# Kernel tuning notes

Hardware: AMD Instinct MI355X
Metric: run time of the kernel (lower is better)

The kernel has to match this reference:

```python
import jax, jax.numpy as jnp
import numpy as np

K = 20
EPS = 1e-5


def _knn_idx(x, k):
    # x: (B, C, N) -> idx (B, N, k) of nearest neighbors (largest negative sq dist)
    xt = jnp.swapaxes(x, 1, 2)                      # (B, N, C)
    inner = -2.0 * jnp.einsum('bnc,bmc->bnm', xt, xt)
    xx = jnp.sum(x * x, axis=1)                      # (B, N)
    pd = -xx[:, :, None] - inner - xx[:, None, :]    # (B, N, N)
    return jax.lax.top_k(pd, k)[1]


def _graph_feature(x, k):
    # x: (B, C, N) -> (B, 2C, N, k): concat(neighbor - center, center)
    idx = _knn_idx(x, k)                             # (B, N, k) int
    xt = jnp.swapaxes(x, 1, 2)                       # (B, N, C)
    neigh = jax.vmap(lambda f, i: f[i])(xt, idx)     # (B, N, k, C)
    center = jnp.broadcast_to(xt[:, :, None, :], neigh.shape)
    feat = jnp.concatenate([neigh - center, center], axis=-1)  # (B, N, k, 2C)
    return jnp.transpose(feat, (0, 3, 1, 2))         # (B, 2C, N, k)


def _bn_lrelu(y, g, b, rm, rv, chan_axis_nd):
    # inference-mode batchnorm per channel (dim 1) followed by LeakyReLU(0.2)
    shp = [1, -1] + [1] * chan_axis_nd
    scale = (g / jnp.sqrt(rv + EPS)).reshape(shp)
    y = (y - rm.reshape(shp)) * scale + b.reshape(shp)
    return jnp.where(y > 0, y, 0.2 * y)


def _edge_block(x, w, g, b, rm, rv):
    f = _graph_feature(x, K)                          # (B, 2C, N, k)
    y = jnp.einsum('oc,bcnk->bonk', w, f)            # conv2d 1x1, no bias
    y = _bn_lrelu(y, g, b, rm, rv, 2)
    return jnp.max(y, axis=-1)                       # max over k -> (B, O, N)


def setup_inputs() -> dict:
    key = jax.random.key(0)
    ks = jax.random.split(key, 32)
    B, N = 8, 4096
    d = {'x': jax.random.normal(ks[0], (B, 1, N), jnp.float32)}
    wshapes = {'w1': (64, 2), 'w2': (64, 128), 'w3': (128, 128), 'w4': (256, 256),
               'w5': (1024, 512), 'wreg': (1, 1024)}
    i = 1
    for name, s in wshapes.items():
        d[name] = jax.random.normal(ks[i], s, jnp.float32) * 0.1
        i += 1
    chans = {'1': 64, '2': 64, '3': 128, '4': 256, '5': 1024}
    for tag, c in chans.items():
        d['g' + tag] = 1.0 + 0.1 * jax.random.normal(ks[i], (c,), jnp.float32); i += 1
        d['b' + tag] = 0.1 * jax.random.normal(ks[i], (c,), jnp.float32); i += 1
        d['rm' + tag] = 0.1 * jax.random.normal(ks[i], (c,), jnp.float32); i += 1
        d['rv' + tag] = jax.random.uniform(ks[i], (c,), jnp.float32, 0.5, 1.5); i += 1
    return d


def reference(x, w1, w2, w3, w4, w5, wreg,
              g1, b1, rm1, rv1, g2, b2, rm2, rv2, g3, b3, rm3, rv3,
              g4, b4, rm4, rv4, g5, b5, rm5, rv5):
    x1 = _edge_block(x, w1, g1, b1, rm1, rv1)        # (B, 64, N)
    x2 = _edge_block(x1, w2, g2, b2, rm2, rv2)       # (B, 64, N)
    x3 = _edge_block(x2, w3, g3, b3, rm3, rv3)       # (B, 128, N)
    x4 = _edge_block(x3, w4, g4, b4, rm4, rv4)       # (B, 256, N)
    h = jnp.concatenate([x1, x2, x3, x4], axis=1)    # (B, 512, N)
    h = jnp.einsum('oc,bcn->bon', w5, h)             # conv1d 1x1 -> (B, 1024, N)
    h = _bn_lrelu(h, g5, b5, rm5, rv5, 1)
    return jnp.einsum('oc,bcn->bon', wreg, h)        # (B, 1, N)
```

## Files before the change

kernel.cpp:

```cpp
#include <hip/hip_runtime.h>
#include <math.h>


constexpr int NPT = 4096;
constexpr int BATCH = 8;
constexpr int PTS = BATCH * NPT;
constexpr float EPS = 1e-5f;
#define KC 16
#define PAD 68
#define PADB 132
#define NEG_INF -3.4e38f

__global__ __launch_bounds__(256) void sqnorm(const float* __restrict__ X,
                                              float* __restrict__ xx, int C) {
    int p = blockIdx.x * 256 + threadIdx.x;
    if (p >= PTS) return;
    float s = 0.f;
    const float* row = X + (size_t)p * C;
    for (int c = 0; c < C; ++c) s = fmaf(row[c], row[c], s);
    xx[p] = s;
}

__global__ __launch_bounds__(256) void pd_sym128(const float* __restrict__ X,
                                                 const float* __restrict__ xx,
                                                 float* __restrict__ pd0,
                                                 int C, int bbase, size_t pdstride) {
    int b = bbase + blockIdx.y;
    float* pd = pd0 + (size_t)blockIdx.y * pdstride;
    int bid = blockIdx.x;
    int ti = 0, rem = bid;
    while (rem >= 32 - ti) { rem -= 32 - ti; ++ti; }
    int tj = ti + rem;
    int rowbase = ti * 128, colbase = tj * 128;

    __shared__ __align__(16) float As[KC][PADB];
    __shared__ __align__(16) float Bs[KC][PADB];
    int tid = threadIdx.x;
    int tx = tid & 15;
    int ty = tid >> 4;
    int p0 = b * NPT;
    int sc4 = (tid & 3) * 4;
    int spt = tid >> 2;
    float acc[2][2][4][4] = {};
    for (int c0 = 0; c0 < C; c0 += KC) {
#pragma unroll
        for (int h = 0; h < 2; ++h) {
            int pt = spt + h * 64;
            float4 av = *(const float4*)&X[(size_t)(p0 + rowbase + pt) * C + c0 + sc4];
            float4 bv = *(const float4*)&X[(size_t)(p0 + colbase + pt) * C + c0 + sc4];
            As[sc4 + 0][pt] = av.x; As[sc4 + 1][pt] = av.y;
            As[sc4 + 2][pt] = av.z; As[sc4 + 3][pt] = av.w;
            Bs[sc4 + 0][pt] = bv.x; Bs[sc4 + 1][pt] = bv.y;
            Bs[sc4 + 2][pt] = bv.z; Bs[sc4 + 3][pt] = bv.w;
        }
        __syncthreads();
#pragma unroll
        for (int cc = 0; cc < KC; ++cc) {
            float4 a0 = *(const float4*)&As[cc][ty * 4];
            float4 a1 = *(const float4*)&As[cc][64 + ty * 4];
            float4 b0 = *(const float4*)&Bs[cc][tx * 4];
            float4 b1 = *(const float4*)&Bs[cc][64 + tx * 4];
            float ar[2][4] = {{a0.x, a0.y, a0.z, a0.w}, {a1.x, a1.y, a1.z, a1.w}};
            float br[2][4] = {{b0.x, b0.y, b0.z, b0.w}, {b1.x, b1.y, b1.z, b1.w}};
#pragma unroll
            for (int rh = 0; rh < 2; ++rh)
#pragma unroll
                for (int i = 0; i < 4; ++i)
#pragma unroll
                    for (int ch = 0; ch < 2; ++ch)
#pragma unroll
                        for (int j = 0; j < 4; ++j)
                            acc[rh][ch][i][j] = fmaf(ar[rh][i], br[ch][j], acc[rh][ch][i][j]);
        }
        __syncthreads();
    }
    float xr[2][4], xm[2][4];
#pragma unroll
    for (int rh = 0; rh < 2; ++rh)
#pragma unroll
        for (int i = 0; i < 4; ++i) xr[rh][i] = xx[p0 + rowbase + rh * 64 + ty * 4 + i];
#pragma unroll
    for (int ch = 0; ch < 2; ++ch)
#pragma unroll
        for (int j = 0; j < 4; ++j) xm[ch][j] = xx[p0 + colbase + ch * 64 + tx * 4 + j];
#pragma unroll
    for (int rh = 0; rh < 2; ++rh)
#pragma unroll
        for (int i = 0; i < 4; ++i) {
            int r = rowbase + rh * 64 + ty * 4 + i;
            float xrv = xr[rh][i];
#pragma unroll
            for (int ch = 0; ch < 2; ++ch) {
                int m = colbase + ch * 64 + tx * 4;
                float4 o;
                o.x = 2.f * acc[rh][ch][i][0] - xrv - xm[ch][0];
                o.y = 2.f * acc[rh][ch][i][1] - xrv - xm[ch][1];
                o.z = 2.f * acc[rh][ch][i][2] - xrv - xm[ch][2];
                o.w = 2.f * acc[rh][ch][i][3] - xrv - xm[ch][3];
                *(float4*)&pd[(size_t)r * NPT + m] = o;
            }
        }
    if (ti != tj) {
#pragma unroll
        for (int ch = 0; ch < 2; ++ch)
#pragma unroll
            for (int j = 0; j < 4; ++j) {
                int m = colbase + ch * 64 + tx * 4 + j;
                float xmv = xm[ch][j];
#pragma unroll
                for (int rh = 0; rh < 2; ++rh) {
                    float4 o;
                    o.x = 2.f * acc[rh][ch][0][j] - xmv - xr[rh][0];
                    o.y = 2.f * acc[rh][ch][1][j] - xmv - xr[rh][1];
                    o.z = 2.f * acc[rh][ch][2][j] - xmv - xr[rh][2];
                    o.w = 2.f * acc[rh][ch][3][j] - xmv - xr[rh][3];
                    *(float4*)&pd[(size_t)m * NPT + rowbase + rh * 64 + ty * 4] = o;
                }
            }
    }
}

__device__ __forceinline__ void topk_core(float (&v)[64], int lane, int b,
                                          int* __restrict__ op) {
    float m1 = NEG_INF, m2 = NEG_INF;
    int j1 = 0, j2 = 0;
#pragma unroll
    for (int j = 0; j < 64; ++j) {
        float vv = v[j];
        bool c1 = vv > m1;
        bool c2 = vv > m2;
        m2 = c1 ? m1 : (c2 ? vv : m2);
        j2 = c1 ? j1 : (c2 ? j : j2);
        m1 = c1 ? vv : m1;
        j1 = c1 ? j : j1;
    }
    bool have2 = true;
    unsigned long long remM = 0ull;
    for (int t = 0; t < 20; ++t) {
        int g1 = ((j1 >> 2) << 8) + (lane << 2) + (j1 & 3);
        float bv = m1; int gi = g1;
#pragma unroll
        for (int s = 1; s < 64; s <<= 1) {
            float ov = __shfl_xor(bv, s);
            int og = __shfl_xor(gi, s);
            if (ov > bv || (ov == bv && og < gi)) { bv = ov; gi = og; }
        }
        if (lane == 0) op[t] = b * NPT + gi;
        bool needscan = false;
        if (gi == g1) {
            remM |= 1ull << j1;
            if (have2) { m1 = m2; j1 = j2; have2 = false; }
            else needscan = true;
        }
        if (__any(needscan)) {
            if (needscan) {
                m1 = NEG_INF; m2 = NEG_INF; j1 = 0; j2 = 0;
#pragma unroll
                for (int j = 0; j < 64; ++j) {
                    bool alive = !((remM >> j) & 1ull);
                    float vv = alive ? v[j] : NEG_INF;
                    bool c1 = vv > m1;
                    bool c2 = vv > m2;
                    m2 = c1 ? m1 : (c2 ? vv : m2);
                    j2 = c1 ? j1 : (c2 ? j : j2);
                    m1 = c1 ? vv : m1;
                    j1 = c1 ? j : j1;
                }
                have2 = true;
            }
        }
    }
}

__global__ __launch_bounds__(256) void topk20(const float* __restrict__ pd0,
                                              int* __restrict__ idxout,
                                              int bbase, size_t pdstride) {
    int b = bbase + blockIdx.y;
    const float* pd = pd0 + (size_t)blockIdx.y * pdstride;
    int row = blockIdx.x * 4 + (threadIdx.x >> 6);
    int lane = threadIdx.x & 63;
    const float4* prow4 = (const float4*)(pd + (size_t)row * NPT);
    float v[64];
#pragma unroll
    for (int q = 0; q < 16; ++q) {
        float4 t = prow4[q * 64 + lane];
        v[q * 4 + 0] = t.x; v[q * 4 + 1] = t.y;
        v[q * 4 + 2] = t.z; v[q * 4 + 3] = t.w;
    }
    topk_core(v, lane, b, idxout + (size_t)(b * NPT + row) * 20);
}

__global__ __launch_bounds__(256) void topk1(const float* __restrict__ X,
                                             const float* __restrict__ xx,
                                             int* __restrict__ idxout) {
    int b = blockIdx.y;
    int row = blockIdx.x * 4 + (threadIdx.x >> 6);
    int lane = threadIdx.x & 63;
    int p0 = b * NPT;
    float xr = X[p0 + row];
    float xxr = xx[p0 + row];
    const float4* xb4 = (const float4*)(X + p0);
    const float4* xxb4 = (const float4*)(xx + p0);
    float v[64];
#pragma unroll
    for (int q = 0; q < 16; ++q) {
        float4 xm = xb4[q * 64 + lane];
        float4 xxm = xxb4[q * 64 + lane];
        v[q * 4 + 0] = (2.f * (xr * xm.x) - xxr) - xxm.x;
        v[q * 4 + 1] = (2.f * (xr * xm.y) - xxr) - xxm.y;
        v[q * 4 + 2] = (2.f * (xr * xm.z) - xxr) - xxm.z;
        v[q * 4 + 3] = (2.f * (xr * xm.w) - xxr) - xxm.w;
    }
    topk_core(v, lane, b, idxout + (size_t)(b * NPT + row) * 20);
}

__global__ __launch_bounds__(256) void ut1(const float* __restrict__ X,
                                           const float* __restrict__ w,
                                           float* __restrict__ U,
                                           float* __restrict__ T) {
    int p = blockIdx.x * 4 + (threadIdx.x >> 6);
    int o = threadIdx.x & 63;
    float xv = X[p];
    float wa = w[o * 2];
    float wt = w[o * 2 + 1] - wa;
    U[(size_t)p * 64 + o] = wa * xv;
    T[(size_t)p * 64 + o] = wt * xv;
}

__global__ __launch_bounds__(256) void ut_gemm(const float* __restrict__ X,
                                               const float* __restrict__ w,
                                               float* __restrict__ U,
                                               float* __restrict__ T,
                                               int C, int O) {
    __shared__ float Xs[KC][PAD];
    __shared__ float Wa[KC][PAD];
    __shared__ float Wt[KC][PAD];
    int tid = threadIdx.x;
    int tx = tid & 15;
    int ty = tid >> 4;
    int pbase = blockIdx.x * 64;
    int obase = blockIdx.y * 64;
    int lc = tid & 15;
    int li = tid >> 4;
    float aU[4][4] = {}, aT[4][4] = {};
    for (int c0 = 0; c0 < C; c0 += KC) {
        int c = c0 + lc;
#pragma unroll
        for (int r = 0; r < 4; ++r) {
            int i = li + r * 16;
            Xs[lc][i] = X[(size_t)(pbase + i) * C + c];
            const float* wrow = w + (size_t)(obase + i) * (2 * C);
            float wa = wrow[c];
            Wa[lc][i] = wa;
            Wt[lc][i] = wrow[C + c] - wa;
        }
        __syncthreads();
#pragma unroll
        for (int cc = 0; cc < KC; ++cc) {
            float xv[4], wav[4], wtv[4];
#pragma unroll
            for (int i = 0; i < 4; ++i) xv[i] = Xs[cc][tx * 4 + i];
#pragma unroll
            for (int j = 0; j < 4; ++j) { wav[j] = Wa[cc][ty * 4 + j]; wtv[j] = Wt[cc][ty * 4 + j]; }
#pragma unroll
            for (int j = 0; j < 4; ++j)
#pragma unroll
                for (int i = 0; i < 4; ++i) {
                    aU[j][i] = fmaf(wav[j], xv[i], aU[j][i]);
                    aT[j][i] = fmaf(wtv[j], xv[i], aT[j][i]);
                }
        }
        __syncthreads();
    }
#pragma unroll
    for (int j = 0; j < 4; ++j)
#pragma unroll
        for (int i = 0; i < 4; ++i) {
            size_t p = pbase + tx * 4 + i;
            int o = obase + ty * 4 + j;
            U[p * O + o] = aU[j][i];
            T[p * O + o] = aT[j][i];
        }
}

__global__ __launch_bounds__(256) void gather_max4(const float* __restrict__ U,
                                                   const float* __restrict__ T,
                                                   const int* __restrict__ idx,
                                                   const float* __restrict__ g,
                                                   const float* __restrict__ bb,
                                                   const float* __restrict__ rm,
                                                   const float* __restrict__ rv,
                                                   float* __restrict__ Xout, int O) {
    int tpp = O / 4;
    int ppb = 256 / tpp;
    int lp = threadIdx.x / tpp;
    int o4 = (threadIdx.x % tpp) * 4;
    int p = blockIdx.x * ppb + lp;
    const int* ip = idx + (size_t)p * 20;
    float4 m = {NEG_INF, NEG_INF, NEG_INF, NEG_INF};
#pragma unroll
    for (int k = 0; k < 20; ++k) {
        int j = ip[k];
        float4 u = *(const float4*)&U[(size_t)j * O + o4];
        m.x = fmaxf(m.x, u.x); m.y = fmaxf(m.y, u.y);
        m.z = fmaxf(m.z, u.z); m.w = fmaxf(m.w, u.w);
    }
    float4 t = *(const float4*)&T[(size_t)p * O + o4];
    float4 gg = *(const float4*)&g[o4];
    float4 bv = *(const float4*)&bb[o4];
    float4 rmv = *(const float4*)&rm[o4];
    float4 rvv = *(const float4*)&rv[o4];
    float4 y;
    y.x = (m.x + t.x - rmv.x) * (gg.x / sqrtf(rvv.x + EPS)) + bv.x;
    y.y = (m.y + t.y - rmv.y) * (gg.y / sqrtf(rvv.y + EPS)) + bv.y;
    y.z = (m.z + t.z - rmv.z) * (gg.z / sqrtf(rvv.z + EPS)) + bv.z;
    y.w = (m.w + t.w - rmv.w) * (gg.w / sqrtf(rvv.w + EPS)) + bv.w;
    y.x = y.x > 0.f ? y.x : 0.2f * y.x;
    y.y = y.y > 0.f ? y.y : 0.2f * y.y;
    y.z = y.z > 0.f ? y.z : 0.2f * y.z;
    y.w = y.w > 0.f ? y.w : 0.2f * y.w;
    *(float4*)&Xout[(size_t)p * O + o4] = y;
}

__global__ __launch_bounds__(256) void head_partial(const float* __restrict__ X1,
                                                    const float* __restrict__ X2,
                                                    const float* __restrict__ X3,
                                                    const float* __restrict__ X4,
                                                    const float* __restrict__ w5,
                                                    const float* __restrict__ wreg,
                                                    const float* __restrict__ g,
                                                    const float* __restrict__ bb,
                                                    const float* __restrict__ rm,
                                                    const float* __restrict__ rv,
                                                    float* __restrict__ partial) {
    __shared__ __align__(16) float Ws[KC][PADB];
    __shared__ __align__(16) float Hs[KC][PADB];
    __shared__ float red[16][PADB];
    int tid = threadIdx.x;
    int tx = tid & 15;
    int ty = tid >> 4;
    int o0 = blockIdx.x * 128;
    int p0 = blockIdx.y * 128;
    int sc4 = (tid & 3) * 4;
    int spt = tid >> 2;
    float acc[2][2][4][4] = {};
    for (int c0 = 0; c0 < 512; c0 += KC) {
        const float* src;
        int coff, Cs;
        if (c0 < 64)       { src = X1; coff = c0;       Cs = 64; }
        else if (c0 < 128) { src = X2; coff = c0 - 64;  Cs = 64; }
        else if (c0 < 256) { src = X3; coff = c0 - 128; Cs = 128; }
        else               { src = X4; coff = c0 - 256; Cs = 256; }
#pragma unroll
        for (int h = 0; h < 2; ++h) {
            int pt = spt + h * 64;
            float4 wv = *(const float4*)&w5[(size_t)(o0 + pt) * 512 + c0 + sc4];
            float4 hv = *(const float4*)&src[(size_t)(p0 + pt) * Cs + coff + sc4];
            Ws[sc4 + 0][pt] = wv.x; Ws[sc4 + 1][pt] = wv.y;
            Ws[sc4 + 2][pt] = wv.z; Ws[sc4 + 3][pt] = wv.w;
            Hs[sc4 + 0][pt] = hv.x; Hs[sc4 + 1][pt] = hv.y;
            Hs[sc4 + 2][pt] = hv.z; Hs[sc4 + 3][pt] = hv.w;
        }
        __syncthreads();
#pragma unroll
        for (int cc = 0; cc < KC; ++cc) {
            float4 a0 = *(const float4*)&Ws[cc][ty * 4];
            float4 a1 = *(const float4*)&Ws[cc][64 + ty * 4];
            float4 b0 = *(const float4*)&Hs[cc][tx * 4];
            float4 b1 = *(const float4*)&Hs[cc][64 + tx * 4];
            float ar[2][4] = {{a0.x, a0.y, a0.z, a0.w}, {a1.x, a1.y, a1.z, a1.w}};
            float br[2][4] = {{b0.x, b0.y, b0.z, b0.w}, {b1.x, b1.y, b1.z, b1.w}};
#pragma unroll
            for (int rh = 0; rh < 2; ++rh)
#pragma unroll
                for (int i = 0; i < 4; ++i)
#pragma unroll
                    for (int ch = 0; ch < 2; ++ch)
#pragma unroll
                        for (int j = 0; j < 4; ++j)
                            acc[rh][ch][i][j] = fmaf(ar[rh][i], br[ch][j], acc[rh][ch][i][j]);
        }
        __syncthreads();
    }
    float pacc[2][4] = {};
#pragma unroll
    for (int rh = 0; rh < 2; ++rh)
#pragma unroll
        for (int i = 0; i < 4; ++i) {
            int o = o0 + rh * 64 + ty * 4 + i;
            float scale = g[o] / sqrtf(rv[o] + EPS);
            float sm = rm[o], sb = bb[o], wr = wreg[o];
#pragma unroll
            for (int ch = 0; ch < 2; ++ch)
#pragma unroll
                for (int j = 0; j < 4; ++j) {
                    float y = (acc[rh][ch][i][j] - sm) * scale + sb;
                    y = y > 0.f ? y : 0.2f * y;
                    pacc[ch][j] = fmaf(wr, y, pacc[ch][j]);
                }
        }
#pragma unroll
    for (int ch = 0; ch < 2; ++ch)
#pragma unroll
        for (int j = 0; j < 4; ++j)
            red[ty][ch * 64 + tx * 4 + j] = pacc[ch][j];
    __syncthreads();
    if (tid < 128) {
        float s = 0.f;
#pragma unroll
        for (int q = 0; q < 16; ++q) s += red[q][tid];
        partial[(size_t)blockIdx.x * PTS + p0 + tid] = s;
    }
}

__global__ __launch_bounds__(256) void head_reduce(const float* __restrict__ partial,
                                                   float* __restrict__ out) {
    int p = blockIdx.x * 256 + threadIdx.x;
    if (p >= PTS) return;
    float s = 0.f;
#pragma unroll
    for (int q = 0; q < 8; ++q) s += partial[(size_t)q * PTS + p];
    out[p] = s;
}

extern "C" void kernel_launch(void* const* d_in, const int* in_sizes, int n_in,
                              void* d_out, int out_size, void* d_ws, size_t ws_size,
                              hipStream_t stream) {
    const float* x    = (const float*)d_in[0];
    const float* w1   = (const float*)d_in[1];
    const float* w2   = (const float*)d_in[2];
    const float* w3   = (const float*)d_in[3];
    const float* w4   = (const float*)d_in[4];
    const float* w5   = (const float*)d_in[5];
    const float* wreg = (const float*)d_in[6];
    const float* bn[5][4];
    for (int t = 0; t < 5; ++t)
        for (int q = 0; q < 4; ++q)
            bn[t][q] = (const float*)d_in[7 + t * 4 + q];
    float* out = (float*)d_out;

    char* ws = (char*)d_ws;
    size_t o_x1  = 0;
    size_t o_x2  = o_x1  + (size_t)PTS * 64 * 4;
    size_t o_x3  = o_x2  + (size_t)PTS * 64 * 4;
    size_t o_x4  = o_x3  + (size_t)PTS * 128 * 4;
    size_t o_idx = o_x4  + (size_t)PTS * 256 * 4;
    size_t o_xx  = o_idx + (size_t)PTS * 20 * 4;
    size_t o_pd  = o_xx  + (size_t)PTS * 4;
    size_t o_u   = o_pd;
    size_t o_t   = o_u   + (size_t)PTS * 256 * 4;
    size_t pdslab = (size_t)NPT * NPT * 4;

    float* X1 = (float*)(ws + o_x1);
    float* X2 = (float*)(ws + o_x2);
    float* X3 = (float*)(ws + o_x3);
    float* X4 = (float*)(ws + o_x4);
    int*   IDX = (int*)(ws + o_idx);
    float* XX = (float*)(ws + o_xx);
    float* PD = (float*)(ws + o_pd);
    float* U  = (float*)(ws + o_u);
    float* T  = (float*)(ws + o_t);
    float* PART = (float*)(ws + o_idx);

    const bool pair = ws_size >= o_pd + 2 * pdslab;
    const int bstep = pair ? 2 : 1;
    const size_t pdstride = pair ? (pdslab / 4) * 0 + (size_t)NPT * NPT : 0;

    auto knn_layer = [&](const float* Xin, int C) {
        for (int b = 0; b < BATCH; b += bstep) {
            pd_sym128<<<dim3(528, bstep), 256, 0, stream>>>(Xin, XX, PD, C, b,
                                                            pair ? (size_t)NPT * NPT : 0);
            topk20<<<dim3(NPT / 4, bstep), 256, 0, stream>>>(PD, IDX, b,
                                                             pair ? (size_t)NPT * NPT : 0);
        }
    };

    sqnorm<<<PTS / 256, 256, 0, stream>>>(x, XX, 1);
    topk1<<<dim3(NPT / 4, BATCH), 256, 0, stream>>>(x, XX, IDX);
    ut1<<<PTS / 4, 256, 0, stream>>>(x, w1, U, T);
    gather_max4<<<PTS * 16 / 256, 256, 0, stream>>>(U, T, IDX,
            bn[0][0], bn[0][1], bn[0][2], bn[0][3], X1, 64);

    sqnorm<<<PTS / 256, 256, 0, stream>>>(X1, XX, 64);
    knn_layer(X1, 64);
    ut_gemm<<<dim3(PTS / 64, 1), 256, 0, stream>>>(X1, w2, U, T, 64, 64);
    gather_max4<<<PTS * 16 / 256, 256, 0, stream>>>(U, T, IDX,
            bn[1][0], bn[1][1], bn[1][2], bn[1][3], X2, 64);

    sqnorm<<<PTS / 256, 256, 0, stream>>>(X2, XX, 64);
    knn_layer(X2, 64);
    ut_gemm<<<dim3(PTS / 64, 2), 256, 0, stream>>>(X2, w3, U, T, 64, 128);
    gather_max4<<<PTS * 32 / 256, 256, 0, stream>>>(U, T, IDX,
            bn[2][0], bn[2][1], bn[2][2], bn[2][3], X3, 128);

    sqnorm<<<PTS / 256, 256, 0, stream>>>(X3, XX, 128);
    knn_layer(X3, 128);
    ut_gemm<<<dim3(PTS / 64, 4), 256, 0, stream>>>(X3, w4, U, T, 128, 256);
    gather_max4<<<PTS * 64 / 256, 256, 0, stream>>>(U, T, IDX,
            bn[3][0], bn[3][1], bn[3][2], bn[3][3], X4, 256);

    head_partial<<<dim3(8, PTS / 128), 256, 0, stream>>>(X1, X2, X3, X4, w5, wreg,
            bn[4][0], bn[4][1], bn[4][2], bn[4][3], PART);
    head_reduce<<<PTS / 256, 256, 0, stream>>>(PART, out);
}
```

Baseline: 2.384 ms.

## Compute pairwise distances with split-bf16 MFMA instead of FP32 FMA

Replaces the FP32 SIMT pairwise inner-product kernel with an MFMA kernel. It splits each feature into bf16 hi and lo parts and uses three bf16 16x16x32 products to approximate FP32 precision. A new sqnorm_cvt kernel writes the hi/lo bf16 copies into the not-yet-used X4 buffer. The aim is to cut the compute cost of the per-batch distance GEMM. The trade-offs are an extra conversion pass, slightly lower precision that could flip near-tied kNN neighbors, and scalar (non-vectorized) stores for the direct-tile output.

```diff
diff --git a/kernel.cpp b/kernel.cpp
--- a/kernel.cpp
+++ b/kernel.cpp
@@ -11,6 +11,14 @@
 #define PADB 132
 #define NEG_INF -3.4e38f
 
+typedef __attribute__((ext_vector_type(8))) short bf16x8;
+typedef __attribute__((ext_vector_type(4))) float f32x4;
+
+__device__ __forceinline__ ushort f2bf(float f) {
+    unsigned u = __float_as_uint(f);
+    return (ushort)((u + 0x7fffu + ((u >> 16) & 1u)) >> 16);
+}
+
 __global__ __launch_bounds__(256) void sqnorm(const float* __restrict__ X,
                                               float* __restrict__ xx, int C) {
     int p = blockIdx.x * 256 + threadIdx.x;
@@ -21,10 +29,32 @@
     xx[p] = s;
 }
 
-__global__ __launch_bounds__(256) void pd_sym128(const float* __restrict__ X,
-                                                 const float* __restrict__ xx,
-                                                 float* __restrict__ pd0,
-                                                 int C, int bbase, size_t pdstride) {
+__global__ __launch_bounds__(256) void sqnorm_cvt(const float* __restrict__ X,
+                                                  float* __restrict__ xx,
+                                                  ushort* __restrict__ Xh,
+                                                  ushort* __restrict__ Xl, int C) {
+    int p = blockIdx.x * 256 + threadIdx.x;
+    if (p >= PTS) return;
+    const float* row = X + (size_t)p * C;
+    ushort* hr = Xh + (size_t)p * C;
+    ushort* lr = Xl + (size_t)p * C;
+    float s = 0.f;
+    for (int c = 0; c < C; ++c) {
+        float v = row[c];
+        s = fmaf(v, v, s);
+        ushort hb = f2bf(v);
+        float hf = __uint_as_float((unsigned)hb << 16);
+        hr[c] = hb;
+        lr[c] = f2bf(v - hf);
+    }
+    xx[p] = s;
+}
+
+__global__ __launch_bounds__(256) void pd_mfma(const ushort* __restrict__ Xh,
+                                               const ushort* __restrict__ Xl,
+                                               const float* __restrict__ xx,
+                                               float* __restrict__ pd0,
+                                               int C, int bbase, size_t pdstride) {
     int b = bbase + blockIdx.y;
     float* pd = pd0 + (size_t)blockIdx.y * pdstride;
     int bid = blockIdx.x;
@@ -32,91 +62,96 @@
     while (rem >= 32 - ti) { rem -= 32 - ti; ++ti; }
     int tj = ti + rem;
     int rowbase = ti * 128, colbase = tj * 128;
-
-    __shared__ __align__(16) float As[KC][PADB];
-    __shared__ __align__(16) float Bs[KC][PADB];
+    int p0 = b * NPT;
+
+    __shared__ ushort Rh[128][40], Rl[128][40], Ch[128][40], Cl[128][40];
+    __shared__ float xxr[128], xxc[128];
     int tid = threadIdx.x;
-    int tx = tid & 15;
-    int ty = tid >> 4;
-    int p0 = b * NPT;
-    int sc4 = (tid & 3) * 4;
-    int spt = tid >> 2;
-    float acc[2][2][4][4] = {};
-    for (int c0 = 0; c0 < C; c0 += KC) {
-#pragma unroll
-        for (int h = 0; h < 2; ++h) {
-            int pt = spt + h * 64;
-            float4 av = *(const float4*)&X[(size_t)(p0 + rowbase + pt) * C + c0 + sc4];
-            float4 bv = *(const float4*)&X[(size_t)(p0 + colbase + pt) * C + c0 + sc4];
-            As[sc4 + 0][pt] = av.x; As[sc4 + 1][pt] = av.y;
-            As[sc4 + 2][pt] = av.z; As[sc4 + 3][pt] = av.w;
-            Bs[sc4 + 0][pt] = bv.x; Bs[sc4 + 1][pt] = bv.y;
-            Bs[sc4 + 2][pt] = bv.z; Bs[sc4 + 3][pt] = bv.w;
-        }
+    int lane = tid & 63, wid = tid >> 6;
+    int wr = wid >> 1, wc = wid & 1;
+
+    if (tid < 128) xxr[tid] = xx[p0 + rowbase + tid];
+    else           xxc[tid - 128] = xx[p0 + colbase + tid - 128];
+
+    const int pt = tid >> 1;
+    const int co = (tid & 1) * 16;
+    size_t rrow = (size_t)(p0 + rowbase + pt) * C;
+    size_t crow = (size_t)(p0 + colbase + pt) * C;
+
+    f32x4 z = {0.f, 0.f, 0.f, 0.f};
+    f32x4 acc[4][4];
+#pragma unroll
+    for (int sr = 0; sr < 4; ++sr)
+#pragma unroll
+        for (int sc = 0; sc < 4; ++sc) acc[sr][sc] = z;
+
+    for (int c0 = 0; c0 < C; c0 += 32) {
+        uint4 vrh0 = *(const uint4*)&Xh[rrow + c0 + co];
+        uint4 vrh1 = *(const uint4*)&Xh[rrow + c0 + co + 8];
+        uint4 vrl0 = *(const uint4*)&Xl[rrow + c0 + co];
+        uint4 vrl1 = *(const uint4*)&Xl[rrow + c0 + co + 8];
+        uint4 vch0 = *(const uint4*)&Xh[crow + c0 + co];
+        uint4 vch1 = *(const uint4*)&Xh[crow + c0 + co + 8];
+        uint4 vcl0 = *(const uint4*)&Xl[crow + c0 + co];
+        uint4 vcl1 = *(const uint4*)&Xl[crow + c0 + co + 8];
         __syncthreads();
-#pragma unroll
-        for (int cc = 0; cc < KC; ++cc) {
-            float4 a0 = *(const float4*)&As[cc][ty * 4];
-            float4 a1 = *(const float4*)&As[cc][64 + ty * 4];
-            float4 b0 = *(const float4*)&Bs[cc][tx * 4];
-            float4 b1 = *(const float4*)&Bs[cc][64 + tx * 4];
-            float ar[2][4] = {{a0.x, a0.y, a0.z, a0.w}, {a1.x, a1.y, a1.z, a1.w}};
-            float br[2][4] = {{b0.x, b0.y, b0.z, b0.w}, {b1.x, b1.y, b1.z, b1.w}};
-#pragma unroll
-            for (int rh = 0; rh < 2; ++rh)
-#pragma unroll
-                for (int i = 0; i < 4; ++i)
-#pragma unroll
-                    for (int ch = 0; ch < 2; ++ch)
-#pragma unroll
-                        for (int j = 0; j < 4; ++j)
-                            acc[rh][ch][i][j] = fmaf(ar[rh][i], br[ch][j], acc[rh][ch][i][j]);
-        }
+        *(uint4*)&Rh[pt][co] = vrh0; *(uint4*)&Rh[pt][co + 8] = vrh1;
+        *(uint4*)&Rl[pt][co] = vrl0; *(uint4*)&Rl[pt][co + 8] = vrl1;
+        *(uint4*)&Ch[pt][co] = vch0; *(uint4*)&Ch[pt][co + 8] = vch1;
+        *(uint4*)&Cl[pt][co] = vcl0; *(uint4*)&Cl[pt][co + 8] = vcl1;
         __syncthreads();
-    }
-    float xr[2][4], xm[2][4];
-#pragma unroll
-    for (int rh = 0; rh < 2; ++rh)
-#pragma unroll
-        for (int i = 0; i < 4; ++i) xr[rh][i] = xx[p0 + rowbase + rh * 64 + ty * 4 + i];
-#pragma unroll
-    for (int ch = 0; ch < 2; ++ch)
-#pragma unroll
-        for (int j = 0; j < 4; ++j) xm[ch][j] = xx[p0 + colbase + ch * 64 + tx * 4 + j];
-#pragma unroll
-    for (int rh = 0; rh < 2; ++rh)
-#pragma unroll
-        for (int i = 0; i < 4; ++i) {
-            int r = rowbase + rh * 64 + ty * 4 + i;
-            float xrv = xr[rh][i];
-#pragma unroll
-            for (int ch = 0; ch < 2; ++ch) {
-                int m = colbase + ch * 64 + tx * 4;
+        bf16x8 ah[4], al[4], bh[4], bl[4];
+#pragma unroll
+        for (int s = 0; s < 4; ++s) {
+            int ar = wr * 64 + s * 16 + (lane & 15);
+            int br = wc * 64 + s * 16 + (lane & 15);
+            int ko = (lane >> 4) * 8;
+            ah[s] = *(const bf16x8*)&Rh[ar][ko];
+            al[s] = *(const bf16x8*)&Rl[ar][ko];
+            bh[s] = *(const bf16x8*)&Ch[br][ko];
+            bl[s] = *(const bf16x8*)&Cl[br][ko];
+        }
+#pragma unroll
+        for (int sr = 0; sr < 4; ++sr)
+#pragma unroll
+            for (int sc = 0; sc < 4; ++sc) {
+                acc[sr][sc] = __builtin_amdgcn_mfma_f32_16x16x32_bf16(ah[sr], bh[sc], acc[sr][sc], 0, 0, 0);
+                acc[sr][sc] = __builtin_amdgcn_mfma_f32_16x16x32_bf16(ah[sr], bl[sc], acc[sr][sc], 0, 0, 0);
+                acc[sr][sc] = __builtin_amdgcn_mfma_f32_16x16x32_bf16(al[sr], bh[sc], acc[sr][sc], 0, 0, 0);
+            }
+    }
+
+    int rl0 = wr * 64 + (lane >> 4) * 4;
+    int ml  = wc * 64 + (lane & 15);
+#pragma unroll
+    for (int sr = 0; sr < 4; ++sr)
+#pragma unroll
+        for (int sc = 0; sc < 4; ++sc) {
+            int mm = ml + sc * 16;
+            float xm = xxc[mm];
+#pragma unroll
+            for (int reg = 0; reg < 4; ++reg) {
+                int rr = rl0 + sr * 16 + reg;
+                float o = 2.f * acc[sr][sc][reg] - xxr[rr] - xm;
+                pd[(size_t)(rowbase + rr) * NPT + colbase + mm] = o;
+            }
+        }
+    if (ti != tj) {
+#pragma unroll
+        for (int sr = 0; sr < 4; ++sr) {
+            int rr0 = rl0 + sr * 16;
+#pragma unroll
+            for (int sc = 0; sc < 4; ++sc) {
+                int mm = ml + sc * 16;
+                float xm = xxc[mm];
                 float4 o;
-                o.x = 2.f * acc[rh][ch][i][0] - xrv - xm[ch][0];
-                o.y = 2.f * acc[rh][ch][i][1] - xrv - xm[ch][1];
-                o.z = 2.f * acc[rh][ch][i][2] - xrv - xm[ch][2];
-                o.w = 2.f * acc[rh][ch][i][3] - xrv - xm[ch][3];
-                *(float4*)&pd[(size_t)r * NPT + m] = o;
+                o.x = 2.f * acc[sr][sc][0] - xm - xxr[rr0 + 0];
+                o.y = 2.f * acc[sr][sc][1] - xm - xxr[rr0 + 1];
+                o.z = 2.f * acc[sr][sc][2] - xm - xxr[rr0 + 2];
+                o.w = 2.f * acc[sr][sc][3] - xm - xxr[rr0 + 3];
+                *(float4*)&pd[(size_t)(colbase + mm) * NPT + rowbase + rr0] = o;
             }
         }
-    if (ti != tj) {
-#pragma unroll
-        for (int ch = 0; ch < 2; ++ch)
-#pragma unroll
-            for (int j = 0; j < 4; ++j) {
-                int m = colbase + ch * 64 + tx * 4 + j;
-                float xmv = xm[ch][j];
-#pragma unroll
-                for (int rh = 0; rh < 2; ++rh) {
-                    float4 o;
-                    o.x = 2.f * acc[rh][ch][0][j] - xmv - xr[rh][0];
-                    o.y = 2.f * acc[rh][ch][1][j] - xmv - xr[rh][1];
-                    o.z = 2.f * acc[rh][ch][2][j] - xmv - xr[rh][2];
-                    o.w = 2.f * acc[rh][ch][3][j] - xmv - xr[rh][3];
-                    *(float4*)&pd[(size_t)m * NPT + rowbase + rh * 64 + ty * 4] = o;
-                }
-            }
     }
 }
 
@@ -450,6 +485,7 @@
     size_t o_u   = o_pd;
     size_t o_t   = o_u   + (size_t)PTS * 256 * 4;
     size_t pdslab = (size_t)NPT * NPT * 4;
+    (void)o_t;
 
     float* X1 = (float*)(ws + o_x1);
     float* X2 = (float*)(ws + o_x2);
@@ -459,19 +495,19 @@
     float* XX = (float*)(ws + o_xx);
     float* PD = (float*)(ws + o_pd);
     float* U  = (float*)(ws + o_u);
-    float* T  = (float*)(ws + o_t);
+    float* T  = (float*)(ws + o_u + (size_t)PTS * 256 * 4);
     float* PART = (float*)(ws + o_idx);
+    ushort* XH = (ushort*)(ws + o_x4);
+    ushort* XL = (ushort*)(ws + o_x4 + (size_t)PTS * 128 * 2);
 
     const bool pair = ws_size >= o_pd + 2 * pdslab;
     const int bstep = pair ? 2 : 1;
-    const size_t pdstride = pair ? (pdslab / 4) * 0 + (size_t)NPT * NPT : 0;
-
-    auto knn_layer = [&](const float* Xin, int C) {
+    const size_t pdstride = pair ? (size_t)NPT * NPT : 0;
+
+    auto knn_layer = [&](int C) {
         for (int b = 0; b < BATCH; b += bstep) {
-            pd_sym128<<<dim3(528, bstep), 256, 0, stream>>>(Xin, XX, PD, C, b,
-                                                            pair ? (size_t)NPT * NPT : 0);
-            topk20<<<dim3(NPT / 4, bstep), 256, 0, stream>>>(PD, IDX, b,
-                                                             pair ? (size_t)NPT * NPT : 0);
+            pd_mfma<<<dim3(528, bstep), 256, 0, stream>>>(XH, XL, XX, PD, C, b, pdstride);
+            topk20<<<dim3(NPT / 4, bstep), 256, 0, stream>>>(PD, IDX, b, pdstride);
         }
     };
 
@@ -481,20 +517,20 @@
     gather_max4<<<PTS * 16 / 256, 256, 0, stream>>>(U, T, IDX,
             bn[0][0], bn[0][1], bn[0][2], bn[0][3], X1, 64);
 
-    sqnorm<<<PTS / 256, 256, 0, stream>>>(X1, XX, 64);
-    knn_layer(X1, 64);
+    sqnorm_cvt<<<PTS / 256, 256, 0, stream>>>(X1, XX, XH, XL, 64);
+    knn_layer(64);
     ut_gemm<<<dim3(PTS / 64, 1), 256, 0, stream>>>(X1, w2, U, T, 64, 64);
     gather_max4<<<PTS * 16 / 256, 256, 0, stream>>>(U, T, IDX,
             bn[1][0], bn[1][1], bn[1][2], bn[1][3], X2, 64);
 
-    sqnorm<<<PTS / 256, 256, 0, stream>>>(X2, XX, 64);
-    knn_layer(X2, 64);
+    sqnorm_cvt<<<PTS / 256, 256, 0, stream>>>(X2, XX, XH, XL, 64);
+    knn_layer(64);
     ut_gemm<<<dim3(PTS / 64, 2), 256, 0, stream>>>(X2, w3, U, T, 64, 128);
     gather_max4<<<PTS * 32 / 256, 256, 0, stream>>>(U, T, IDX,
             bn[2][0], bn[2][1], bn[2][2], bn[2][3], X3, 128);
 
-    sqnorm<<<PTS / 256, 256, 0, stream>>>(X3, XX, 128);
-    knn_layer(X3, 128);
+    sqnorm_cvt<<<PTS / 256, 256, 0, stream>>>(X3, XX, XH, XL, 128);
+    knn_layer(128);
     ut_gemm<<<dim3(PTS / 64, 4), 256, 0, stream>>>(X3, w4, U, T, 128, 256);
     gather_max4<<<PTS * 64 / 256, 256, 0, stream>>>(U, T, IDX,
             bn[3][0], bn[3][1], bn[3][2], bn[3][3], X4, 256);
```

Result: no change. 2.407 ms (+1.0%).
